# Optimization experiments

Measured on AMD Instinct MI355X. Metric: run time of the kernel, lower is better.

Reference implementation:

```python
import jax, jax.numpy as jnp
import numpy as np

D_MODEL = 1024
NUM_HEADS = 16


def setup_inputs() -> dict:
    key = jax.random.key(0)
    ks = jax.random.split(key, 6)
    B, N, L, C = 16, 1024, 120, D_MODEL
    s = 0.02
    return {
        "x": jax.random.normal(ks[0], (B, N, C), jnp.float32),
        "cond": jax.random.normal(ks[1], (B, L, C), jnp.float32),
        "mask": jax.random.randint(ks[2], (B, L), 0, 2, jnp.int32),
        "Wq": jax.random.normal(ks[3], (C, C), jnp.float32) * s,
        "bq": jnp.zeros((C,), jnp.float32),
        "Wkv": jax.random.normal(ks[4], (2 * C, C), jnp.float32) * s,
        "bkv": jnp.zeros((2 * C,), jnp.float32),
        "Wp": jax.random.normal(ks[5], (C, C), jnp.float32) * s,
        "bp": jnp.zeros((C,), jnp.float32),
    }


def reference(x, cond, mask, Wq, bq, Wkv, bkv, Wp, bp):
    B, N, C = x.shape
    H = NUM_HEADS
    Dh = C // H
    scale = Dh ** (-0.5)
    # q: (B,H,N,Dh)
    q = (x @ Wq.T + bq).reshape(B, N, H, Dh).transpose(0, 2, 1, 3)
    # kv: (2,B,H,L,Dh)
    L = cond.shape[1]
    kv = (cond @ Wkv.T + bkv).reshape(B, L, 2, H, Dh).transpose(2, 0, 3, 1, 4)
    k, v = kv[0], kv[1]
    # attention scores (B,H,N,L)
    attn = jnp.einsum("bhnd,bhld->bhnl", q, k) * scale
    attn = jnp.where(mask[:, None, None, :] == 0, -jnp.inf, attn)
    attn = jax.nn.softmax(attn, axis=-1)
    out = jnp.einsum("bhnl,bhld->bhnd", attn, v)  # (B,H,N,Dh)
    out = out.transpose(0, 2, 1, 3).reshape(B, N, C)
    return out @ Wp.T + bp
```

## Files before the change

### kernel.cpp

```cpp
#include <hip/hip_runtime.h>

typedef unsigned short u16;
typedef unsigned int u32;
typedef float f32x4 __attribute__((ext_vector_type(4)));
typedef __bf16 bf16x8 __attribute__((ext_vector_type(8)));
typedef u32 u32x4 __attribute__((ext_vector_type(4)));
typedef u16 u16x4 __attribute__((ext_vector_type(4)));

#define NB 16
#define NSEQ 1024
#define NL 120
#define NLP 128
#define NC 1024
#define NH 16
#define NDH 64
#define KSP 72
#define VTP 136

__device__ __forceinline__ u16 f2bf(float f) {
  u32 u = __float_as_uint(f);
  return (u16)((u + 0x7fffu + ((u >> 16) & 1u)) >> 16);
}

__device__ __forceinline__ void gld_lds16(const void* g, void* l) {
  __builtin_amdgcn_global_load_lds(
      (const __attribute__((address_space(1))) void*)g,
      (__attribute__((address_space(3))) void*)l, 16, 0, 0);
}

#define SBAR()                               \
  do {                                       \
    __builtin_amdgcn_sched_barrier(0);       \
    __builtin_amdgcn_s_barrier();            \
    __builtin_amdgcn_sched_barrier(0);       \
  } while (0)
#define VMW(n)                                          \
  do {                                                  \
    __builtin_amdgcn_sched_barrier(0);                  \
    asm volatile("s_waitcnt vmcnt(" #n ")" ::: "memory"); \
  } while (0)

__global__ __launch_bounds__(256) void cast_all(
    const float* __restrict__ x, u16* __restrict__ xb,
    const float* __restrict__ cond, u16* __restrict__ condb,
    const float* __restrict__ Wq, u16* __restrict__ Wqb,
    const float* __restrict__ Wkv, u16* __restrict__ Wkvb,
    const float* __restrict__ Wp, u16* __restrict__ Wpb) {
  int bk = blockIdx.x;
  const float* src;
  u16* dst;
  if (bk < 16384) { src = x; dst = xb; }
  else if (bk < 18304) { src = cond; dst = condb; bk -= 16384; }
  else if (bk < 19328) { src = Wq; dst = Wqb; bk -= 18304; }
  else if (bk < 21376) { src = Wkv; dst = Wkvb; bk -= 19328; }
  else { src = Wp; dst = Wpb; bk -= 21376; }
  size_t i = ((size_t)bk * 256 + threadIdx.x) * 4;
  f32x4 v = *(const f32x4*)(src + i);
  u16x4 o;
  o.x = f2bf(v.x); o.y = f2bf(v.y); o.z = f2bf(v.z); o.w = f2bf(v.w);
  *(u16x4*)(dst + i) = o;
}

template <bool OUT_F32>
__global__ __launch_bounds__(256) void gemm_bt(
    const u16* __restrict__ A, const u16* __restrict__ Bt,
    const float* __restrict__ bias, void* __restrict__ Cout,
    int M, int Nn, int K) {
  __shared__ u16 As[128 * 32];
  __shared__ u16 Bs[128 * 32];
  const int mt = M >> 7;
  const int bm = (int)blockIdx.x % mt;
  const int bn = (int)blockIdx.x / mt;
  const int m0 = bm << 7, n0 = bn << 7;
  const int tid = threadIdx.x;
  const int w = tid >> 6, lane = tid & 63;
  const int wm = (w & 1) << 6, wn = (w >> 1) << 6;
  const int quad = lane >> 4, l15 = lane & 15;

  f32x4 acc[4][4];
#pragma unroll
  for (int i = 0; i < 4; ++i)
#pragma unroll
    for (int j = 0; j < 4; ++j) acc[i][j] = (f32x4){0.f, 0.f, 0.f, 0.f};

  const int r0 = tid >> 2;
  const int cb = ((((tid & 3) - (r0 >> 1)) & 3)) << 3;
  const u16* aP = A + (size_t)(m0 + r0) * K + cb;
  const u16* bP = Bt + (size_t)(n0 + r0) * K + cb;
  u16* asDst = &As[r0 * 32 + ((tid & 3) << 3)];
  u16* bsDst = &Bs[r0 * 32 + ((tid & 3) << 3)];

  const int sw = ((quad + (l15 >> 1)) & 3) << 3;

  for (int k0 = 0; k0 < K; k0 += 32) {
    __syncthreads();
    gld_lds16(aP + k0, asDst);
    gld_lds16(aP + (size_t)64 * K + k0, asDst + 64 * 32);
    gld_lds16(bP + k0, bsDst);
    gld_lds16(bP + (size_t)64 * K + k0, bsDst + 64 * 32);
    __syncthreads();

    bf16x8 af[4], bfr[4];
#pragma unroll
    for (int i = 0; i < 4; ++i)
      af[i] = *(const bf16x8*)&As[(wm + i * 16 + l15) * 32 + sw];
#pragma unroll
    for (int j = 0; j < 4; ++j)
      bfr[j] = *(const bf16x8*)&Bs[(wn + j * 16 + l15) * 32 + sw];
#pragma unroll
    for (int i = 0; i < 4; ++i)
#pragma unroll
      for (int j = 0; j < 4; ++j)
        acc[i][j] =
            __builtin_amdgcn_mfma_f32_16x16x32_bf16(af[i], bfr[j], acc[i][j], 0, 0, 0);
  }

#pragma unroll
  for (int j = 0; j < 4; ++j) {
    const int col = n0 + wn + j * 16 + l15;
    const float bv = bias[col];
#pragma unroll
    for (int i = 0; i < 4; ++i) {
      const int row = m0 + wm + i * 16 + quad * 4;
#pragma unroll
      for (int r = 0; r < 4; ++r) {
        const float v = acc[i][j][r] + bv;
        if (OUT_F32)
          ((float*)Cout)[(size_t)(row + r) * Nn + col] = v;
        else
          ((u16*)Cout)[(size_t)(row + r) * Nn + col] = f2bf(v);
      }
    }
  }
}

template <bool OUT_F32>
__global__ __launch_bounds__(512, 2) void gemm256(
    const u16* __restrict__ A, const u16* __restrict__ Bt,
    const float* __restrict__ bias, void* __restrict__ Cout,
    int M, int Nn, int K) {
  __shared__ u16 S[2][2][2][8192];

  const int bid = (int)blockIdx.x;
  const int nwg = (M >> 8) * (Nn >> 8);
  const int cpx = nwg >> 3;
  const int swz = (bid & 7) * cpx + (bid >> 3);
  const int mt = M >> 8;
  const int bm = swz % mt, bn = swz / mt;
  const int m0 = bm << 8, n0 = bn << 8;

  const int tid = threadIdx.x;
  const int w = tid >> 6, lane = tid & 63;
  const int quad = lane >> 4, l15 = lane & 15;
  const int wr = w & 1, wc = w >> 1;

  const int srow = tid >> 3;
  const int xoff = (((tid & 7) ^ (srow & 7)) << 3);
  const u16* aB0 = A + (size_t)(m0 + srow) * K + xoff;
  const u16* bB0 = Bt + (size_t)(n0 + srow) * K + xoff;
  const size_t rowK64 = (size_t)64 * K;
  const size_t rowK128 = (size_t)128 * K;

  auto STAGE = [&](int ab, int buf, int half, int t) {
    const u16* g = (ab ? bB0 : aB0) + half * rowK128 + t * 64;
    u16* d = &S[ab][buf][half][0] + tid * 8;
    gld_lds16(g, d);
    gld_lds16(g + rowK64, d + 4096);
  };

  const int c0 = ((quad << 4) ^ ((l15 & 7) << 4));
  const int c1 = c0 ^ 64;
  const int arow = (wr * 64 + l15) * 128;
  const int brow = (wc * 32 + l15) * 128;

  bf16x8 af[4][2], bfl[2][2], bfh[2][2];
  auto LDA = [&](int buf, int rh) {
    const char* base = (const char*)&S[0][buf][rh][0] + arow;
#pragma unroll
    for (int f = 0; f < 4; ++f) {
      af[f][0] = *(const bf16x8*)(base + f * 2048 + c0);
      af[f][1] = *(const bf16x8*)(base + f * 2048 + c1);
    }
  };
  auto LDB = [&](bf16x8(&bf)[2][2], int buf, int ch) {
    const char* base = (const char*)&S[1][buf][ch][0] + brow;
#pragma unroll
    for (int g = 0; g < 2; ++g) {
      bf[g][0] = *(const bf16x8*)(base + g * 2048 + c0);
      bf[g][1] = *(const bf16x8*)(base + g * 2048 + c1);
    }
  };

  f32x4 a_ll[4][2], a_lh[4][2], a_hh[4][2], a_hl[4][2];
#pragma unroll
  for (int f = 0; f < 4; ++f)
#pragma unroll
    for (int g = 0; g < 2; ++g) {
      a_ll[f][g] = (f32x4){0.f, 0.f, 0.f, 0.f};
      a_lh[f][g] = (f32x4){0.f, 0.f, 0.f, 0.f};
      a_hh[f][g] = (f32x4){0.f, 0.f, 0.f, 0.f};
      a_hl[f][g] = (f32x4){0.f, 0.f, 0.f, 0.f};
    }

  auto MM = [&](f32x4(&acc)[4][2], bf16x8(&bf)[2][2]) {
    __builtin_amdgcn_s_setprio(1);
#pragma unroll
    for (int f = 0; f < 4; ++f)
#pragma unroll
      for (int g = 0; g < 2; ++g) {
        acc[f][g] = __builtin_amdgcn_mfma_f32_16x16x32_bf16(af[f][0], bf[g][0],
                                                            acc[f][g], 0, 0, 0);
        acc[f][g] = __builtin_amdgcn_mfma_f32_16x16x32_bf16(af[f][1], bf[g][1],
                                                            acc[f][g], 0, 0, 0);
      }
    __builtin_amdgcn_s_setprio(0);
  };

  const int NT = K >> 6;
  const int NIT = K >> 7;

  STAGE(0, 0, 0, 0); STAGE(0, 0, 1, 0); STAGE(1, 0, 0, 0); STAGE(1, 0, 1, 0);
  STAGE(0, 1, 0, 1); STAGE(1, 1, 1, 1);
  VMW(4);
  SBAR();

#pragma unroll 1
  for (int it = 0; it < NIT; ++it) {
    const int t1 = 2 * it + 1;
    int t2 = 2 * it + 2; if (t2 > NT - 1) t2 = NT - 1;
    int t3 = 2 * it + 3; if (t3 > NT - 1) t3 = NT - 1;
    LDA(0, 0); LDB(bfl, 0, 0); STAGE(1, 1, 0, t1);
    SBAR(); MM(a_ll, bfl); SBAR();
    LDB(bfh, 0, 1); STAGE(0, 1, 1, t1);
    SBAR(); MM(a_lh, bfh); VMW(6); SBAR();
    LDA(0, 1); STAGE(0, 0, 0, t2);
    SBAR(); MM(a_hh, bfh); SBAR();
    STAGE(1, 0, 1, t2);
    SBAR(); MM(a_hl, bfl); VMW(6); SBAR();
    LDA(1, 0); LDB(bfl, 1, 0); STAGE(1, 0, 0, t2);
    SBAR(); MM(a_ll, bfl); SBAR();
    LDB(bfh, 1, 1); STAGE(0, 0, 1, t2);
    SBAR(); MM(a_lh, bfh); VMW(6); SBAR();
    LDA(1, 1); STAGE(0, 1, 0, t3);
    SBAR(); MM(a_hh, bfh); SBAR();
    STAGE(1, 1, 1, t3);
    SBAR(); MM(a_hl, bfl); VMW(6); SBAR();
  }

  auto EPI = [&](f32x4(&acc)[4][2], int rh, int ch) {
#pragma unroll
    for (int g = 0; g < 2; ++g) {
      const int col = n0 + ch * 128 + wc * 32 + g * 16 + l15;
      const float bv = bias[col];
#pragma unroll
      for (int f = 0; f < 4; ++f) {
        const int row = m0 + rh * 128 + wr * 64 + f * 16 + quad * 4;
#pragma unroll
        for (int r = 0; r < 4; ++r) {
          const float v = acc[f][g][r] + bv;
          if (OUT_F32)
            ((float*)Cout)[(size_t)(row + r) * Nn + col] = v;
          else
            ((u16*)Cout)[(size_t)(row + r) * Nn + col] = f2bf(v);
        }
      }
    }
  };
  EPI(a_ll, 0, 0); EPI(a_lh, 0, 1); EPI(a_hh, 1, 1); EPI(a_hl, 1, 0);
}

__global__ __launch_bounds__(256) void attn(
    const u16* __restrict__ Qb, const u16* __restrict__ KVb,
    const int* __restrict__ mask, u16* __restrict__ Ob) {
  __shared__ u16 Ks[NLP * KSP];
  __shared__ u16 Vt[NDH * VTP];
  __shared__ float mb[NLP];
  __shared__ u16 pb[4][16 * VTP];

  const int chunk = (int)blockIdx.x & 3;
  const int h = ((int)blockIdx.x >> 2) & 15;
  const int b = (int)blockIdx.x >> 6;
  const int tid = threadIdx.x;
  const int w = tid >> 6, lane = tid & 63;
  const int quad = lane >> 4, l15 = lane & 15;
  const u16* kvbase = KVb + (size_t)b * NL * 2 * NC;

  for (int i = tid; i < NLP * 8; i += 256) {
    const int l = i >> 3, c8 = (i & 7) * 8;
    u32x4 z = {0u, 0u, 0u, 0u};
    u32x4 v = (l < NL) ? *(const u32x4*)(kvbase + (size_t)l * 2 * NC + h * NDH + c8) : z;
    *(u32x4*)&Ks[l * KSP + c8] = v;
  }
  u16* vstage = &pb[0][0];
  for (int i = tid; i < NL * 8; i += 256) {
    const int l = i >> 3, c8 = (i & 7) * 8;
    *(u32x4*)&vstage[l * NDH + c8] =
        *(const u32x4*)(kvbase + (size_t)l * 2 * NC + NC + h * NDH + c8);
  }
  for (int i = tid; i < NLP; i += 256)
    mb[i] = (i < NL && mask[b * NL + i] != 0) ? 0.0f : -1e30f;
  __syncthreads();
  {
    const int d = tid & 63;
#pragma unroll
    for (int it2 = 0; it2 < 8; ++it2) {
      const int l4 = (tid >> 6) + it2 * 4;
      u16x4 vv;
      if (l4 < 30) {
        vv.x = vstage[(l4 * 4 + 0) * NDH + d];
        vv.y = vstage[(l4 * 4 + 1) * NDH + d];
        vv.z = vstage[(l4 * 4 + 2) * NDH + d];
        vv.w = vstage[(l4 * 4 + 3) * NDH + d];
      } else {
        vv = (u16x4){0, 0, 0, 0};
      }
      *(u16x4*)&Vt[d * VTP + l4 * 4] = vv;
    }
  }
  __syncthreads();

  const float scale = 0.125f;
  const u16* qbase = Qb + (size_t)(b * NSEQ + chunk * 256 + l15) * NC + h * NDH + quad * 8;
  bf16x8 a0 = *(const bf16x8*)(qbase + (size_t)(0 * 64 + w * 16) * NC);
  bf16x8 a1 = *(const bf16x8*)(qbase + (size_t)(0 * 64 + w * 16) * NC + 32);

  for (int it = 0; it < 4; ++it) {
    const int q0 = chunk * 256 + it * 64 + w * 16;
    const int itn = (it + 1) & 3;
    const u16* qn = qbase + (size_t)(itn * 64 + w * 16) * NC;
    const bf16x8 n0 = *(const bf16x8*)qn;
    const bf16x8 n1 = *(const bf16x8*)(qn + 32);

    f32x4 s[8];
#pragma unroll
    for (int kt = 0; kt < 8; ++kt) {
      const u16* kb = &Ks[(kt * 16 + l15) * KSP + quad * 8];
      const bf16x8 b0 = *(const bf16x8*)kb;
      const bf16x8 b1 = *(const bf16x8*)(kb + 32);
      f32x4 t = {0.f, 0.f, 0.f, 0.f};
      t = __builtin_amdgcn_mfma_f32_16x16x32_bf16(a0, b0, t, 0, 0, 0);
      t = __builtin_amdgcn_mfma_f32_16x16x32_bf16(a1, b1, t, 0, 0, 0);
      s[kt] = t;
    }
#pragma unroll
    for (int kt = 0; kt < 8; ++kt) {
      const float mbv = mb[kt * 16 + l15];
#pragma unroll
      for (int r = 0; r < 4; ++r) s[kt][r] = s[kt][r] * scale + mbv;
    }
    float sum[4];
#pragma unroll
    for (int r = 0; r < 4; ++r) {
      float m = s[0][r];
#pragma unroll
      for (int kt = 1; kt < 8; ++kt) m = fmaxf(m, s[kt][r]);
      m = fmaxf(m, __shfl_xor(m, 1));
      m = fmaxf(m, __shfl_xor(m, 2));
      m = fmaxf(m, __shfl_xor(m, 4));
      m = fmaxf(m, __shfl_xor(m, 8));
      float su = 0.f;
#pragma unroll
      for (int kt = 0; kt < 8; ++kt) {
        s[kt][r] = __expf(s[kt][r] - m);
        su += s[kt][r];
      }
      su += __shfl_xor(su, 1);
      su += __shfl_xor(su, 2);
      su += __shfl_xor(su, 4);
      su += __shfl_xor(su, 8);
      sum[r] = su;
    }
#pragma unroll
    for (int r = 0; r < 4; ++r) {
      const float inv = 1.0f / sum[r];
#pragma unroll
      for (int kt = 0; kt < 8; ++kt)
        pb[w][(quad * 4 + r) * VTP + kt * 16 + l15] = f2bf(s[kt][r] * inv);
    }
#pragma unroll
    for (int ntl = 0; ntl < 4; ++ntl) {
      f32x4 o = {0.f, 0.f, 0.f, 0.f};
#pragma unroll
      for (int kt = 0; kt < 4; ++kt) {
        const bf16x8 pa = *(const bf16x8*)&pb[w][l15 * VTP + kt * 32 + quad * 8];
        const bf16x8 vb = *(const bf16x8*)&Vt[(ntl * 16 + l15) * VTP + kt * 32 + quad * 8];
        o = __builtin_amdgcn_mfma_f32_16x16x32_bf16(pa, vb, o, 0, 0, 0);
      }
#pragma unroll
      for (int r = 0; r < 4; ++r)
        Ob[(size_t)(b * NSEQ + q0 + quad * 4 + r) * NC + h * NDH + ntl * 16 + l15] =
            f2bf(o[r]);
    }
    a0 = n0;
    a1 = n1;
  }
}

extern "C" void kernel_launch(void* const* d_in, const int* in_sizes, int n_in,
                              void* d_out, int out_size, void* d_ws, size_t ws_size,
                              hipStream_t stream) {
  const float* x = (const float*)d_in[0];
  const float* cond = (const float*)d_in[1];
  const int* mask = (const int*)d_in[2];
  const float* Wq = (const float*)d_in[3];
  const float* bq = (const float*)d_in[4];
  const float* Wkv = (const float*)d_in[5];
  const float* bkv = (const float*)d_in[6];
  const float* Wp = (const float*)d_in[7];
  const float* bp = (const float*)d_in[8];

  char* ws = (char*)d_ws;
  u16* xb = (u16*)(ws + 0);
  u16* condb = (u16*)(ws + 33554432);
  u16* Wqb = (u16*)(ws + 37486592);
  u16* Wkvb = (u16*)(ws + 39583744);
  u16* Wpb = (u16*)(ws + 43778048);
  u16* Qb = (u16*)(ws + 45875200);
  u16* KVb = (u16*)(ws + 79429632);
  u16* Ob = xb;

  cast_all<<<22400, 256, 0, stream>>>(x, xb, cond, condb, Wq, Wqb, Wkv, Wkvb, Wp, Wpb);

  gemm256<false><<<256, 512, 0, stream>>>(xb, Wqb, bq, Qb, 16384, 1024, 1024);
  gemm_bt<false><<<15 * 16, 256, 0, stream>>>(condb, Wkvb, bkv, KVb, 1920, 2048, 1024);
  attn<<<1024, 256, 0, stream>>>(Qb, KVb, mask, Ob);
  gemm256<true><<<256, 512, 0, stream>>>(Ob, Wpb, bp, d_out, 16384, 1024, 1024);
}
```

Baseline: 278.6 us.

## Double-buffer MFMA register fragments and halve barriers in gemm256 main loop

Rewrites the gemm256 main loop so LDS fragment loads for the next sub-tile go into alternate register sets (afA/afB, blA/blB, bhA/bhB) and overlap with the MFMAs of the current sub-tile. This roughly halves the workgroup barriers per step. It also changes the XCD-aware block swizzle so each XCD owns a contiguous band of M tiles. The cost is higher VGPR pressure, which with launch bounds (512,2) could cause spills. The last iteration also issues a prefetch LDS read that is never used.

```diff
diff --git a/kernel.cpp b/kernel.cpp
--- a/kernel.cpp
+++ b/kernel.cpp
@@ -39,6 +39,7 @@
     __builtin_amdgcn_sched_barrier(0);                  \
     asm volatile("s_waitcnt vmcnt(" #n ")" ::: "memory"); \
   } while (0)
+#define SB0() __builtin_amdgcn_sched_barrier(0)
 
 __global__ __launch_bounds__(256) void cast_all(
     const float* __restrict__ x, u16* __restrict__ xb,
@@ -142,11 +143,11 @@
   __shared__ u16 S[2][2][2][8192];
 
   const int bid = (int)blockIdx.x;
-  const int nwg = (M >> 8) * (Nn >> 8);
-  const int cpx = nwg >> 3;
-  const int swz = (bid & 7) * cpx + (bid >> 3);
   const int mt = M >> 8;
-  const int bm = swz % mt, bn = swz / mt;
+  const int mpx = mt >> 3;
+  const int xcd = bid & 7, idx = bid >> 3;
+  const int bm = xcd * mpx + (idx % mpx);
+  const int bn = idx / mpx;
   const int m0 = bm << 8, n0 = bn << 8;
 
   const int tid = threadIdx.x;
@@ -173,21 +174,21 @@
   const int arow = (wr * 64 + l15) * 128;
   const int brow = (wc * 32 + l15) * 128;
 
-  bf16x8 af[4][2], bfl[2][2], bfh[2][2];
-  auto LDA = [&](int buf, int rh) {
+  bf16x8 afA[4][2], afB[4][2], blA[2][2], blB[2][2], bhA[2][2], bhB[2][2];
+  auto LDA_TO = [&](bf16x8(&dst)[4][2], int buf, int rh) {
     const char* base = (const char*)&S[0][buf][rh][0] + arow;
 #pragma unroll
     for (int f = 0; f < 4; ++f) {
-      af[f][0] = *(const bf16x8*)(base + f * 2048 + c0);
-      af[f][1] = *(const bf16x8*)(base + f * 2048 + c1);
+      dst[f][0] = *(const bf16x8*)(base + f * 2048 + c0);
+      dst[f][1] = *(const bf16x8*)(base + f * 2048 + c1);
     }
   };
-  auto LDB = [&](bf16x8(&bf)[2][2], int buf, int ch) {
+  auto LDB_TO = [&](bf16x8(&dst)[2][2], int buf, int ch) {
     const char* base = (const char*)&S[1][buf][ch][0] + brow;
 #pragma unroll
     for (int g = 0; g < 2; ++g) {
-      bf[g][0] = *(const bf16x8*)(base + g * 2048 + c0);
-      bf[g][1] = *(const bf16x8*)(base + g * 2048 + c1);
+      dst[g][0] = *(const bf16x8*)(base + g * 2048 + c0);
+      dst[g][1] = *(const bf16x8*)(base + g * 2048 + c1);
     }
   };
 
@@ -202,7 +203,7 @@
       a_hl[f][g] = (f32x4){0.f, 0.f, 0.f, 0.f};
     }
 
-  auto MM = [&](f32x4(&acc)[4][2], bf16x8(&bf)[2][2]) {
+  auto MM = [&](f32x4(&acc)[4][2], bf16x8(&af)[4][2], bf16x8(&bf)[2][2]) {
     __builtin_amdgcn_s_setprio(1);
 #pragma unroll
     for (int f = 0; f < 4; ++f)
@@ -223,28 +224,44 @@
   STAGE(0, 1, 0, 1); STAGE(1, 1, 1, 1);
   VMW(4);
   SBAR();
+  LDA_TO(afA, 0, 0); LDB_TO(blA, 0, 0);
+  SB0();
 
 #pragma unroll 1
   for (int it = 0; it < NIT; ++it) {
     const int t1 = 2 * it + 1;
     int t2 = 2 * it + 2; if (t2 > NT - 1) t2 = NT - 1;
     int t3 = 2 * it + 3; if (t3 > NT - 1) t3 = NT - 1;
-    LDA(0, 0); LDB(bfl, 0, 0); STAGE(1, 1, 0, t1);
-    SBAR(); MM(a_ll, bfl); SBAR();
-    LDB(bfh, 0, 1); STAGE(0, 1, 1, t1);
-    SBAR(); MM(a_lh, bfh); VMW(6); SBAR();
-    LDA(0, 1); STAGE(0, 0, 0, t2);
-    SBAR(); MM(a_hh, bfh); SBAR();
-    STAGE(1, 0, 1, t2);
-    SBAR(); MM(a_hl, bfl); VMW(6); SBAR();
-    LDA(1, 0); LDB(bfl, 1, 0); STAGE(1, 0, 0, t2);
-    SBAR(); MM(a_ll, bfl); SBAR();
-    LDB(bfh, 1, 1); STAGE(0, 0, 1, t2);
-    SBAR(); MM(a_lh, bfh); VMW(6); SBAR();
-    LDA(1, 1); STAGE(0, 1, 0, t3);
-    SBAR(); MM(a_hh, bfh); SBAR();
-    STAGE(1, 1, 1, t3);
-    SBAR(); MM(a_hl, bfl); VMW(6); SBAR();
+    STAGE(1, 1, 0, t1);
+    SBAR();
+    LDB_TO(bhA, 0, 1); SB0();
+    MM(a_ll, afA, blA);
+    STAGE(0, 1, 1, t1); VMW(6);
+    SBAR();
+    LDA_TO(afB, 0, 1); SB0();
+    MM(a_lh, afA, bhA);
+    STAGE(0, 0, 0, t2);
+    SBAR();
+    MM(a_hh, afB, bhA);
+    STAGE(1, 0, 1, t2); VMW(6);
+    SBAR();
+    LDA_TO(afA, 1, 0); LDB_TO(blB, 1, 0); SB0();
+    MM(a_hl, afB, blA);
+    STAGE(1, 0, 0, t2);
+    SBAR();
+    LDB_TO(bhB, 1, 1); SB0();
+    MM(a_ll, afA, blB);
+    STAGE(0, 0, 1, t2); VMW(6);
+    SBAR();
+    LDA_TO(afB, 1, 1); SB0();
+    MM(a_lh, afA, bhB);
+    STAGE(0, 1, 0, t3);
+    SBAR();
+    MM(a_hh, afB, bhB);
+    STAGE(1, 1, 1, t3); VMW(6);
+    SBAR();
+    LDA_TO(afA, 0, 0); LDB_TO(blA, 0, 0); SB0();
+    MM(a_hl, afB, blB);
   }
 
   auto EPI = [&](f32x4(&acc)[4][2], int rh, int ch) {
```

Measured after the change: 276.9 us. About the same (-0.6%).
